# Optimization experiments

Hardware: AMD Instinct MI355X
Metric: run time of the kernel (lower is better)

## Reference

```python
import jax, jax.numpy as jnp
import numpy as np

B, S, IN, OUT, H, M = 16, 512, 512, 512, 8, 4
HF = OUT // H  # head_feats = 64


def setup_inputs() -> dict:
    key = jax.random.key(0)
    ks = jax.random.split(key, 12)
    std = 0.02
    queries = jax.random.normal(ks[0], (B, S, IN), jnp.float32)
    keys = jax.random.normal(ks[1], (B, S, IN), jnp.float32)
    timespans = jax.random.uniform(ks[2], (B, S), jnp.float32)
    # causal mask tiled over heads*batch, matching [H*B, S, S] score shape
    attention_masks = jnp.broadcast_to(jnp.tril(jnp.ones((S, S), jnp.float32)), (H * B, S, S))
    event_marks = jax.random.uniform(ks[3], (H * B, 1, S, M), jnp.float32)
    Wq = std * jax.random.normal(ks[4], (IN, OUT), jnp.float32)
    Wk = std * jax.random.normal(ks[5], (IN, OUT), jnp.float32)
    Wv = std * jax.random.normal(ks[6], (IN, OUT), jnp.float32)
    Wt = std * jax.random.normal(ks[7], (IN, OUT), jnp.float32)
    Wi = std * jax.random.normal(ks[8], (HF + 1, M * HF), jnp.float32)  # fc_i weight
    bi = jnp.zeros((M * HF,), jnp.float32)                               # fc_i bias
    weight_i = std * jax.random.normal(ks[9], (M, HF), jnp.float32)
    scale_i = jnp.zeros((M,), jnp.float32)
    return {"queries": queries, "keys": keys, "timespans": timespans,
            "attention_masks": attention_masks, "event_marks": event_marks,
            "Wq": Wq, "Wk": Wk, "Wv": Wv, "Wt": Wt, "Wi": Wi, "bi": bi,
            "weight_i": weight_i, "scale_i": scale_i}


def reference(queries, keys, timespans, attention_masks, event_marks,
              Wq, Wk, Wv, Wt, Wi, bi, weight_i, scale_i):
    # torch's cat(chunk(X, H, dim=2), dim=0) == [B,S,H,HF] -> [H,B,S,HF] -> flat h*B+b
    def split_heads(X):
        return X.reshape(B, S, H, HF).transpose(2, 0, 1, 3)  # [H,B,S,HF]

    Q = split_heads(queries @ Wq)
    K = split_heads(keys @ Wk)
    V = split_heads(keys @ Wv)
    T = split_heads(keys @ Wt)

    scores = jnp.einsum('hbqf,hbkf->hbqk', Q, K) / jnp.sqrt(jnp.float32(OUT))
    mask = attention_masks.reshape(H, B, S, S)
    scores = jnp.where(mask == 0.0, jnp.float32(-2 ** 32 + 1), scores)
    attn = jax.nn.softmax(scores, axis=-1)  # [H,B,Sq,Sk]

    E = jnp.einsum('hbqk,hbkf->hbqf', attn, T)  # events fed to intensity net

    # --- Hawkes intensities ---
    ts = jnp.broadcast_to(timespans[None, :, :, None], (H, B, S, 1))
    mu = jax.nn.sigmoid(jnp.concatenate([E, ts], axis=-1) @ Wi + bi)  # [H,B,S,M*HF]
    mu = mu.reshape(H, B, S, M, HF)  # chunk over marks along feature dim
    scale = jnp.exp(scale_i)  # [M]
    lam = jnp.einsum('hbsmf,mf->hbsm', mu, weight_i) / scale
    lam = scale * jnp.log1p(jnp.exp(lam))  # scaled softplus, [H,B,S,M]

    # mark_inty[h,b,q,k] = sum_m lam[h,b,q,m] * event_marks[h,b,k,m]
    em = event_marks.reshape(H, B, S, M)
    mark_inty = jnp.einsum('hbqm,hbkm->hbqk', lam, em)

    out = jnp.einsum('hbqk,hbkf->hbqf', attn * mark_inty, V)
    out = out.transpose(1, 2, 0, 3).reshape(B, S, OUT) + queries[..., :OUT]
    all_mark_inty = lam.reshape(H * B, S, M)
    return out, all_mark_inty
```

## Files before the change

kernel.cpp:

```cpp
#include <hip/hip_runtime.h>
#include <math.h>

typedef __attribute__((ext_vector_type(8))) short short8;
typedef __attribute__((ext_vector_type(4))) float f32x4;

static __device__ __forceinline__ unsigned short f2bf(float f) {
  unsigned int u = __float_as_uint(f);
  u += 0x7FFFu + ((u >> 16) & 1u);
  return (unsigned short)(u >> 16);
}

static __device__ __forceinline__ void cp16(void* lds, const void* g) {
  __builtin_amdgcn_global_load_lds((const __attribute__((address_space(1))) void*)g,
                                   (__attribute__((address_space(3))) void*)lds,
                                   16, 0, 0);
}

__global__ __launch_bounds__(256) void convert_k(
    const float* __restrict__ qin, const float* __restrict__ kin,
    const float* __restrict__ Wq, const float* __restrict__ Wk,
    const float* __restrict__ Wv, const float* __restrict__ Wt,
    const float* __restrict__ Wi,
    unsigned short* __restrict__ qbf, unsigned short* __restrict__ kbf,
    unsigned short* __restrict__ Wb, unsigned short* __restrict__ WiF)
{
  __shared__ unsigned short tr[64 * 68];
  const int blk = blockIdx.x, tid = threadIdx.x;
  if (blk < 8192) {
    const float* src = (blk < 4096) ? qin : kin;
    unsigned short* dst = (blk < 4096) ? qbf : kbf;
    int i = ((blk & 4095) * 256 + tid) * 4;
    float4 v = *(const float4*)(src + i);
    ushort4 o;
    o.x = f2bf(v.x); o.y = f2bf(v.y); o.z = f2bf(v.z); o.w = f2bf(v.w);
    *(ushort4*)(dst + i) = o;
  } else if (blk < 8448) {
    int t = blk - 8192;
    int which = t >> 6, tile = t & 63;
    int r0 = (tile >> 3) << 6, c0 = (tile & 7) << 6;
    const float* W = (which == 0) ? Wq : (which == 1) ? Wk : (which == 2) ? Wv : Wt;
    const int rr = tid >> 4, cc = (tid & 15) << 2;
#pragma unroll
    for (int u = 0; u < 4; ++u) {
      int r = rr + u * 16;
      float4 v = *(const float4*)(W + (size_t)(r0 + r) * 512 + c0 + cc);
      tr[(cc + 0) * 68 + r] = f2bf(v.x);
      tr[(cc + 1) * 68 + r] = f2bf(v.y);
      tr[(cc + 2) * 68 + r] = f2bf(v.z);
      tr[(cc + 3) * 68 + r] = f2bf(v.w);
    }
    __syncthreads();
    unsigned short* dst = Wb + which * 262144;
#pragma unroll
    for (int u = 0; u < 4; ++u) {
      int c = rr + u * 16;
      ushort4 o = *(const ushort4*)&tr[c * 68 + cc];
      *(ushort4*)(dst + (size_t)(c0 + c) * 512 + r0 + cc) = o;
    }
  } else {
    int e = (blk - 8448) * 256 + tid;
    int j = e & 7, ll = (e >> 3) & 63, r = e >> 9;
    int kk = r % 3, nt = r / 3;
    int col = nt * 16 + (ll & 15);
    int k = kk * 32 + (ll >> 4) * 8 + j;
    float val = (k < 64) ? Wi[k * 256 + col] : ((k == 64) ? Wi[16384 + col] : 0.0f);
    WiF[e] = f2bf(val);
  }
}

__global__ __launch_bounds__(256) void proj_mfma(
    const unsigned short* __restrict__ qin_bf, const unsigned short* __restrict__ kin_bf,
    const unsigned short* __restrict__ Wb,
    unsigned short* __restrict__ Qg, unsigned short* __restrict__ Kg,
    unsigned short* __restrict__ Vt, unsigned short* __restrict__ Tt)
{
  const int which = blockIdx.z;
  const unsigned short* A = (which == 0) ? qin_bf : kin_bf;
  const unsigned short* W = Wb + which * 262144;
  const int row0 = blockIdx.x * 128;
  const int col0 = blockIdx.y * 128;
  const int tid = threadIdx.x;
  const int wv = tid >> 6, l = tid & 63;
  const int quad = l >> 4, lc = l & 15;
  const int wm = wv >> 1, wn = wv & 1;

  __shared__ unsigned short Asm[128 * 32];
  __shared__ unsigned short Bsm[128 * 32];

  f32x4 acc[4][4] = {};
  const int c0 = tid, c1 = tid + 256;

  for (int k0 = 0; k0 < 512; k0 += 32) {
    __syncthreads();
    cp16(&Asm[c0 * 8], A + (size_t)(row0 + (c0 >> 2)) * 512 + k0 + (c0 & 3) * 8);
    cp16(&Asm[c1 * 8], A + (size_t)(row0 + (c1 >> 2)) * 512 + k0 + (c1 & 3) * 8);
    cp16(&Bsm[c0 * 8], W + (size_t)(col0 + (c0 >> 2)) * 512 + k0 + (c0 & 3) * 8);
    cp16(&Bsm[c1 * 8], W + (size_t)(col0 + (c1 >> 2)) * 512 + k0 + (c1 & 3) * 8);
    __syncthreads();
    short8 a[4], b[4];
#pragma unroll
    for (int mi = 0; mi < 4; ++mi)
      a[mi] = *(const short8*)&Asm[(wm * 64 + mi * 16 + lc) * 32 + quad * 8];
#pragma unroll
    for (int nj = 0; nj < 4; ++nj)
      b[nj] = *(const short8*)&Bsm[(wn * 64 + nj * 16 + lc) * 32 + quad * 8];
#pragma unroll
    for (int mi = 0; mi < 4; ++mi)
#pragma unroll
      for (int nj = 0; nj < 4; ++nj)
        acc[mi][nj] = __builtin_amdgcn_mfma_f32_16x16x32_bf16(a[mi], b[nj], acc[mi][nj], 0, 0, 0);
  }

  const int h = (col0 >> 6) + wn;
  const int bidx = row0 >> 9;
  const int hb = h * 16 + bidx;
  if (which < 2) {
    unsigned short* C = (which == 0) ? Qg : Kg;
    const float os = (which == 0) ? 0.044194173824159216f : 1.0f;
#pragma unroll
    for (int mi = 0; mi < 4; ++mi) {
      int sbase = (row0 & 511) + wm * 64 + mi * 16 + quad * 4;
#pragma unroll
      for (int nj = 0; nj < 4; ++nj) {
        size_t base = (size_t)hb * 32768 + (size_t)sbase * 64 + nj * 16 + lc;
#pragma unroll
        for (int reg = 0; reg < 4; ++reg)
          C[base + (size_t)reg * 64] = f2bf(acc[mi][nj][reg] * os);
      }
    }
  } else {
    unsigned short* C = (which == 2) ? Vt : Tt;
    unsigned short* scr = wn ? Bsm : Asm;
    const int sb = (row0 & 511) + wm * 64;
    __syncthreads();
#pragma unroll
    for (int round = 0; round < 2; ++round) {
      if (wm == round) {
#pragma unroll
        for (int mi = 0; mi < 4; ++mi)
#pragma unroll
          for (int nj = 0; nj < 4; ++nj)
#pragma unroll
            for (int reg = 0; reg < 4; ++reg) {
              int f = nj * 16 + lc, s = mi * 16 + quad * 4 + reg;
              int g = (s >> 3) ^ (f & 7);
              scr[f * 64 + g * 8 + (s & 7)] = f2bf(acc[mi][nj][reg]);
            }
#pragma unroll
        for (int it = 0; it < 8; ++it) {
          int fl = it * 8 + (l >> 3);
          int gg = (l & 7) ^ (fl & 7);
          short8 v = *(const short8*)&scr[fl * 64 + gg * 8];
          *(short8*)(C + (size_t)hb * 32768 + (size_t)fl * 512 + sb + (l & 7) * 8) = v;
        }
      }
      __syncthreads();
    }
  }
}

__global__ __launch_bounds__(256, 3) void attn_fused(
    const unsigned short* __restrict__ Qg, const unsigned short* __restrict__ Kg,
    const unsigned short* __restrict__ Vtg, const unsigned short* __restrict__ Ttg,
    const unsigned short* __restrict__ WiF,
    const float* __restrict__ bi, const float* __restrict__ wim,
    const float* __restrict__ sci, const float* __restrict__ tsp,
    const float* __restrict__ em, const float* __restrict__ queries,
    float* __restrict__ out, float* __restrict__ lamout)
{
  const int hb = blockIdx.x;
  const int qt = 7 - blockIdx.y;
  const int q0 = qt << 6;
  const int tid = threadIdx.x, wv = tid >> 6, l = tid & 63;
  const int quad = l >> 4, lc = l & 15;
  const int xg = lc & 7;

  __shared__ unsigned short Qs[4096];
  __shared__ unsigned short Ks[4096];
  __shared__ unsigned short TVs[4096];
  __shared__ unsigned short Wl[4][1536];
  __shared__ float emS[256];

  const int e1 = tid + 256;
  const int sr0 = tid >> 3, sg0 = (tid & 7) ^ (sr0 & 7);
  const int sr1 = e1 >> 3,  sg1 = (e1 & 7) ^ (sr1 & 7);
  const int sqk0 = sr0 * 64 + sg0 * 8,  sqk1 = sr1 * 64 + sg1 * 8;
  const int stv0 = sr0 * 512 + sg0 * 8, stv1 = sr1 * 512 + sg1 * 8;

  const int gqbase = q0 + wv * 16 + quad * 4;

  const unsigned short* Qbase = Qg + (size_t)hb * 32768 + q0 * 64;
  cp16(&Qs[tid * 8], Qbase + sqk0);
  cp16(&Qs[e1 * 8], Qbase + sqk1);

  f32x4 Eacc[4] = {};
  float lsum[4] = {0.f, 0.f, 0.f, 0.f};

  for (int kt = 0; kt <= qt; ++kt) {
    const int k0 = kt << 6;
    __syncthreads();
    const unsigned short* Kbase = Kg + (size_t)hb * 32768 + k0 * 64;
    cp16(&Ks[tid * 8], Kbase + sqk0);
    cp16(&Ks[e1 * 8], Kbase + sqk1);
    const unsigned short* Tbase = Ttg + (size_t)hb * 32768 + k0;
    cp16(&TVs[tid * 8], Tbase + stv0);
    cp16(&TVs[e1 * 8], Tbase + stv1);
    __syncthreads();

    f32x4 sc[4] = {};
#pragma unroll
    for (int kk = 0; kk < 2; ++kk) {
      short8 a = *(const short8*)&Qs[(wv * 16 + lc) * 64 + ((kk * 4 + quad) ^ xg) * 8];
#pragma unroll
      for (int nj = 0; nj < 4; ++nj) {
        short8 b = *(const short8*)&Ks[(nj * 16 + lc) * 64 + ((kk * 4 + quad) ^ xg) * 8];
        sc[nj] = __builtin_amdgcn_mfma_f32_16x16x32_bf16(a, b, sc[nj], 0, 0, 0);
      }
    }
    const bool diag = (kt == qt);
#pragma unroll
    for (int nj = 0; nj < 4; ++nj) {
      int col = nj * 16 + lc;
#pragma unroll
      for (int reg = 0; reg < 4; ++reg) {
        float pv = __expf(sc[nj][reg]);
        if (diag && (k0 + col) > (gqbase + reg)) pv = 0.0f;
        lsum[reg] += pv;
        int row = quad * 4 + reg;
        int gp = (nj * 2 + (lc >> 3)) ^ (row & 7);
        Wl[wv][row * 96 + gp * 8 + (lc & 7)] = f2bf(pv);
      }
    }
#pragma unroll
    for (int kk = 0; kk < 2; ++kk) {
      short8 a = *(const short8*)&Wl[wv][lc * 96 + ((kk * 4 + quad) ^ xg) * 8];
#pragma unroll
      for (int fj = 0; fj < 4; ++fj) {
        short8 b = *(const short8*)&TVs[(fj * 16 + lc) * 64 + ((kk * 4 + quad) ^ xg) * 8];
        Eacc[fj] = __builtin_amdgcn_mfma_f32_16x16x32_bf16(a, b, Eacc[fj], 0, 0, 0);
      }
    }
  }

  float inv[4];
#pragma unroll
  for (int reg = 0; reg < 4; ++reg) {
    float s = lsum[reg];
#pragma unroll
    for (int off = 1; off < 16; off <<= 1) s += __shfl_xor(s, off);
    inv[reg] = 1.0f / s;
  }

#pragma unroll
  for (int reg = 0; reg < 4; ++reg) {
    int row = quad * 4 + reg;
    unsigned short* rp = &Wl[wv][row * 96];
#pragma unroll
    for (int fj = 0; fj < 4; ++fj) {
      int gp = (fj * 2 + (lc >> 3)) ^ (row & 7);
      rp[gp * 8 + (lc & 7)] = f2bf(Eacc[fj][reg] * inv[reg]);
    }
    float tsv = (lc == 0) ? tsp[(hb & 15) * 512 + gqbase + reg] : 0.0f;
    int gt = 8 + ((lc >> 3) ^ (row & 3));
    rp[gt * 8 + (lc & 7)] = f2bf(tsv);
    int gz = 8 + ((2 + (lc >> 3)) ^ (row & 3));
    rp[gz * 8 + (lc & 7)] = 0;
  }

  short8 ia[3];
  ia[0] = *(const short8*)&Wl[wv][lc * 96 + ((0 + quad) ^ xg) * 8];
  ia[1] = *(const short8*)&Wl[wv][lc * 96 + ((4 + quad) ^ xg) * 8];
  ia[2] = *(const short8*)&Wl[wv][lc * 96 + (8 + (quad ^ (lc & 3))) * 8];
  float lam4[4][4] = {};
#pragma unroll
  for (int nt = 0; nt < 16; ++nt) {
    f32x4 iacc = {};
#pragma unroll
    for (int kk = 0; kk < 3; ++kk) {
      short8 b = *(const short8*)(WiF + ((nt * 3 + kk) * 64 + l) * 8);
      iacc = __builtin_amdgcn_mfma_f32_16x16x32_bf16(ia[kk], b, iacc, 0, 0, 0);
    }
    float bvv = bi[nt * 16 + lc];
    float wmv = wim[nt * 16 + lc];
#pragma unroll
    for (int reg = 0; reg < 4; ++reg) {
      float mu = 1.0f / (1.0f + __expf(-(iacc[reg] + bvv)));
      lam4[reg][nt >> 2] += mu * wmv;
    }
  }
#pragma unroll
  for (int m = 0; m < 4; ++m) {
    float scv = __expf(sci[m]);
#pragma unroll
    for (int reg = 0; reg < 4; ++reg) {
      float s = lam4[reg][m];
#pragma unroll
      for (int off = 1; off < 16; off <<= 1) s += __shfl_xor(s, off);
      float z = s / scv;
      float sp = (z > 20.0f) ? z : log1pf(__expf(z));
      lam4[reg][m] = scv * sp;
    }
  }
  if (lc < 4) {
#pragma unroll
    for (int reg = 0; reg < 4; ++reg) {
      float v = (lc == 0) ? lam4[reg][0] : (lc == 1) ? lam4[reg][1]
              : (lc == 2) ? lam4[reg][2] : lam4[reg][3];
      lamout[((size_t)hb * 512 + gqbase + reg) * 4 + lc] = v;
    }
  }

  f32x4 Oacc[4] = {};
  for (int kt = 0; kt <= qt; ++kt) {
    const int k0 = kt << 6;
    __syncthreads();
    const unsigned short* Kbase = Kg + (size_t)hb * 32768 + k0 * 64;
    cp16(&Ks[tid * 8], Kbase + sqk0);
    cp16(&Ks[e1 * 8], Kbase + sqk1);
    const unsigned short* Vbase = Vtg + (size_t)hb * 32768 + k0;
    cp16(&TVs[tid * 8], Vbase + stv0);
    cp16(&TVs[e1 * 8], Vbase + stv1);
    emS[tid] = em[(size_t)hb * 2048 + k0 * 4 + tid];
    __syncthreads();

    f32x4 sc[4] = {};
#pragma unroll
    for (int kk = 0; kk < 2; ++kk) {
      short8 a = *(const short8*)&Qs[(wv * 16 + lc) * 64 + ((kk * 4 + quad) ^ xg) * 8];
#pragma unroll
      for (int nj = 0; nj < 4; ++nj) {
        short8 b = *(const short8*)&Ks[(nj * 16 + lc) * 64 + ((kk * 4 + quad) ^ xg) * 8];
        sc[nj] = __builtin_amdgcn_mfma_f32_16x16x32_bf16(a, b, sc[nj], 0, 0, 0);
      }
    }
    const bool diag = (kt == qt);
#pragma unroll
    for (int nj = 0; nj < 4; ++nj) {
      int col = nj * 16 + lc;
      float4 emv = *(const float4*)&emS[col * 4];
#pragma unroll
      for (int reg = 0; reg < 4; ++reg) {
        float pv = (diag && (k0 + col) > (gqbase + reg))
                       ? 0.0f : __expf(sc[nj][reg]) * inv[reg];
        float mk = lam4[reg][0] * emv.x + lam4[reg][1] * emv.y +
                   lam4[reg][2] * emv.z + lam4[reg][3] * emv.w;
        int row = quad * 4 + reg;
        int gp = (nj * 2 + (lc >> 3)) ^ (row & 7);
        Wl[wv][row * 96 + gp * 8 + (lc & 7)] = f2bf(pv * mk);
      }
    }
#pragma unroll
    for (int kk = 0; kk < 2; ++kk) {
      short8 a = *(const short8*)&Wl[wv][lc * 96 + ((kk * 4 + quad) ^ xg) * 8];
#pragma unroll
      for (int fj = 0; fj < 4; ++fj) {
        short8 b = *(const short8*)&TVs[(fj * 16 + lc) * 64 + ((kk * 4 + quad) ^ xg) * 8];
        Oacc[fj] = __builtin_amdgcn_mfma_f32_16x16x32_bf16(a, b, Oacc[fj], 0, 0, 0);
      }
    }
  }

  const int h = hb >> 4, bidx = hb & 15;
#pragma unroll
  for (int reg = 0; reg < 4; ++reg) {
    size_t o = (size_t)bidx * 262144 + (size_t)(gqbase + reg) * 512 + h * 64 + lc;
#pragma unroll
    for (int fj = 0; fj < 4; ++fj)
      out[o + fj * 16] = Oacc[fj][reg] + queries[o + fj * 16];
  }
}

extern "C" void kernel_launch(void* const* d_in, const int* in_sizes, int n_in,
                              void* d_out, int out_size, void* d_ws, size_t ws_size,
                              hipStream_t stream)
{
  (void)in_sizes; (void)n_in; (void)out_size; (void)ws_size;
  const float* queries = (const float*)d_in[0];
  const float* keys    = (const float*)d_in[1];
  const float* tsp     = (const float*)d_in[2];
  const float* em      = (const float*)d_in[4];
  const float* Wq      = (const float*)d_in[5];
  const float* Wk      = (const float*)d_in[6];
  const float* Wv      = (const float*)d_in[7];
  const float* Wt      = (const float*)d_in[8];
  const float* Wi      = (const float*)d_in[9];
  const float* bi      = (const float*)d_in[10];
  const float* wim     = (const float*)d_in[11];
  const float* sci     = (const float*)d_in[12];
  float* out = (float*)d_out;

  char* w = (char*)d_ws;
  unsigned short* Qg     = (unsigned short*)(w + 0);
  unsigned short* Kg     = (unsigned short*)(w + 8388608);
  unsigned short* Vt     = (unsigned short*)(w + 16777216);
  unsigned short* Tt     = (unsigned short*)(w + 25165824);
  unsigned short* qin_bf = (unsigned short*)(w + 33554432);
  unsigned short* kin_bf = (unsigned short*)(w + 41943040);
  unsigned short* Wb     = (unsigned short*)(w + 50331648);
  unsigned short* WiF    = (unsigned short*)(w + 52428800);

  convert_k<<<8544, 256, 0, stream>>>(queries, keys, Wq, Wk, Wv, Wt, Wi,
                                      qin_bf, kin_bf, Wb, WiF);
  proj_mfma<<<dim3(64, 4, 4), 256, 0, stream>>>(qin_bf, kin_bf, Wb, Qg, Kg, Vt, Tt);
  attn_fused<<<dim3(128, 8), 256, 0, stream>>>(Qg, Kg, Vt, Tt, WiF, bi, wim, sci,
                                               tsp, em, queries, out,
                                               out + 4194304);
}
```

Before: 319.4 us.

## Enlarge attention query tile to 128 rows with double-buffered K/T/V loads

The fused attention kernel now handles 128 query rows per block, two 16-row tiles per wave, so each K/T/V tile loaded into LDS serves twice as many queries. Q fragments are kept in registers, and K/T/V/em tiles are double-buffered so the next tile's async load overlaps the current tile's compute, cutting one barrier per iteration. The grid halves and blocks are ordered largest-first to balance causal work. In exchange, LDS use and register pressure grow (launch bounds drop to 2 blocks per SM), fewer blocks are in flight, and diagonal masking is now checked on every tile.

```diff
diff --git a/kernel.cpp b/kernel.cpp
--- a/kernel.cpp
+++ b/kernel.cpp
@@ -159,7 +159,7 @@
   }
 }
 
-__global__ __launch_bounds__(256, 3) void attn_fused(
+__global__ __launch_bounds__(256, 2) void attn_fused(
     const unsigned short* __restrict__ Qg, const unsigned short* __restrict__ Kg,
     const unsigned short* __restrict__ Vtg, const unsigned short* __restrict__ Ttg,
     const unsigned short* __restrict__ WiF,
@@ -169,17 +169,19 @@
     float* __restrict__ out, float* __restrict__ lamout)
 {
   const int hb = blockIdx.x;
-  const int qt = 7 - blockIdx.y;
-  const int q0 = qt << 6;
+  const int y = blockIdx.y;
+  const int qb = (y == 0) ? 3 : (y == 1) ? 2 : (y == 2) ? 0 : 1;
+  const int q0 = qb << 7;
+  const int kts = 2 * qb + 2;
   const int tid = threadIdx.x, wv = tid >> 6, l = tid & 63;
   const int quad = l >> 4, lc = l & 15;
   const int xg = lc & 7;
 
-  __shared__ unsigned short Qs[4096];
-  __shared__ unsigned short Ks[4096];
-  __shared__ unsigned short TVs[4096];
-  __shared__ unsigned short Wl[4][1536];
-  __shared__ float emS[256];
+  __shared__ unsigned short Qs[8192];
+  __shared__ unsigned short Ks[2][4096];
+  __shared__ unsigned short TVs[2][4096];
+  __shared__ unsigned short Wl[4][3072];
+  __shared__ float emS[2][256];
 
   const int e1 = tid + 256;
   const int sr0 = tid >> 3, sg0 = (tid & 7) ^ (sr0 & 7);
@@ -187,186 +189,238 @@
   const int sqk0 = sr0 * 64 + sg0 * 8,  sqk1 = sr1 * 64 + sg1 * 8;
   const int stv0 = sr0 * 512 + sg0 * 8, stv1 = sr1 * 512 + sg1 * 8;
 
-  const int gqbase = q0 + wv * 16 + quad * 4;
+  const unsigned short* KgB = Kg + (size_t)hb * 32768;
+  const unsigned short* TgB = Ttg + (size_t)hb * 32768;
+  const unsigned short* VgB = Vtg + (size_t)hb * 32768;
 
   const unsigned short* Qbase = Qg + (size_t)hb * 32768 + q0 * 64;
-  cp16(&Qs[tid * 8], Qbase + sqk0);
-  cp16(&Qs[e1 * 8], Qbase + sqk1);
-
-  f32x4 Eacc[4] = {};
-  float lsum[4] = {0.f, 0.f, 0.f, 0.f};
-
-  for (int kt = 0; kt <= qt; ++kt) {
+#pragma unroll
+  for (int u = 0; u < 4; ++u) {
+    int e = tid + u * 256;
+    int r = e >> 3, g = (e & 7) ^ (r & 7);
+    cp16(&Qs[e * 8], Qbase + r * 64 + g * 8);
+  }
+  cp16(&Ks[0][tid * 8], KgB + sqk0);
+  cp16(&Ks[0][e1 * 8], KgB + sqk1);
+  cp16(&TVs[0][tid * 8], TgB + stv0);
+  cp16(&TVs[0][e1 * 8], TgB + stv1);
+  __syncthreads();
+
+  short8 aq[2][2];
+#pragma unroll
+  for (int rt = 0; rt < 2; ++rt)
+#pragma unroll
+    for (int kk = 0; kk < 2; ++kk)
+      aq[rt][kk] = *(const short8*)&Qs[(wv * 32 + rt * 16 + lc) * 64 + ((kk * 4 + quad) ^ xg) * 8];
+
+  f32x4 Eacc[2][4] = {};
+  float lsum[2][4] = {};
+
+  for (int kt = 0; kt < kts; ++kt) {
+    const int cur = kt & 1, nxt = cur ^ 1;
     const int k0 = kt << 6;
-    __syncthreads();
-    const unsigned short* Kbase = Kg + (size_t)hb * 32768 + k0 * 64;
-    cp16(&Ks[tid * 8], Kbase + sqk0);
-    cp16(&Ks[e1 * 8], Kbase + sqk1);
-    const unsigned short* Tbase = Ttg + (size_t)hb * 32768 + k0;
-    cp16(&TVs[tid * 8], Tbase + stv0);
-    cp16(&TVs[e1 * 8], Tbase + stv1);
-    __syncthreads();
-
-    f32x4 sc[4] = {};
-#pragma unroll
-    for (int kk = 0; kk < 2; ++kk) {
-      short8 a = *(const short8*)&Qs[(wv * 16 + lc) * 64 + ((kk * 4 + quad) ^ xg) * 8];
+    if (kt + 1 < kts) {
+      const int k1 = (kt + 1) << 6;
+      cp16(&Ks[nxt][tid * 8], KgB + k1 * 64 + sqk0);
+      cp16(&Ks[nxt][e1 * 8], KgB + k1 * 64 + sqk1);
+      cp16(&TVs[nxt][tid * 8], TgB + k1 + stv0);
+      cp16(&TVs[nxt][e1 * 8], TgB + k1 + stv1);
+    }
+    f32x4 sc[2][4] = {};
+#pragma unroll
+    for (int kk = 0; kk < 2; ++kk)
 #pragma unroll
       for (int nj = 0; nj < 4; ++nj) {
-        short8 b = *(const short8*)&Ks[(nj * 16 + lc) * 64 + ((kk * 4 + quad) ^ xg) * 8];
-        sc[nj] = __builtin_amdgcn_mfma_f32_16x16x32_bf16(a, b, sc[nj], 0, 0, 0);
-      }
-    }
-    const bool diag = (kt == qt);
-#pragma unroll
-    for (int nj = 0; nj < 4; ++nj) {
-      int col = nj * 16 + lc;
+        short8 b = *(const short8*)&Ks[cur][(nj * 16 + lc) * 64 + ((kk * 4 + quad) ^ xg) * 8];
+        sc[0][nj] = __builtin_amdgcn_mfma_f32_16x16x32_bf16(aq[0][kk], b, sc[0][nj], 0, 0, 0);
+        sc[1][nj] = __builtin_amdgcn_mfma_f32_16x16x32_bf16(aq[1][kk], b, sc[1][nj], 0, 0, 0);
+      }
+#pragma unroll
+    for (int rt = 0; rt < 2; ++rt) {
+      const int gq = q0 + wv * 32 + rt * 16 + quad * 4;
+#pragma unroll
+      for (int nj = 0; nj < 4; ++nj) {
+        int col = nj * 16 + lc;
+#pragma unroll
+        for (int reg = 0; reg < 4; ++reg) {
+          float pv = __expf(sc[rt][nj][reg]);
+          if (k0 + col > gq + reg) pv = 0.0f;
+          lsum[rt][reg] += pv;
+          int row = rt * 16 + quad * 4 + reg;
+          int gp = (nj * 2 + (lc >> 3)) ^ (row & 7);
+          Wl[wv][row * 96 + gp * 8 + (lc & 7)] = f2bf(pv);
+        }
+      }
+    }
+#pragma unroll
+    for (int rt = 0; rt < 2; ++rt)
+#pragma unroll
+      for (int kk = 0; kk < 2; ++kk) {
+        short8 a = *(const short8*)&Wl[wv][(rt * 16 + lc) * 96 + ((kk * 4 + quad) ^ xg) * 8];
+#pragma unroll
+        for (int fj = 0; fj < 4; ++fj) {
+          short8 b = *(const short8*)&TVs[cur][(fj * 16 + lc) * 64 + ((kk * 4 + quad) ^ xg) * 8];
+          Eacc[rt][fj] = __builtin_amdgcn_mfma_f32_16x16x32_bf16(a, b, Eacc[rt][fj], 0, 0, 0);
+        }
+      }
+    __syncthreads();
+  }
+
+  float inv[2][4];
+#pragma unroll
+  for (int rt = 0; rt < 2; ++rt)
+#pragma unroll
+    for (int reg = 0; reg < 4; ++reg) {
+      float s = lsum[rt][reg];
+#pragma unroll
+      for (int off = 1; off < 16; off <<= 1) s += __shfl_xor(s, off);
+      inv[rt][reg] = 1.0f / s;
+    }
+
+#pragma unroll
+  for (int rt = 0; rt < 2; ++rt)
+#pragma unroll
+    for (int reg = 0; reg < 4; ++reg) {
+      int row = rt * 16 + quad * 4 + reg;
+      int gq = q0 + wv * 32 + rt * 16 + quad * 4;
+      unsigned short* rp = &Wl[wv][row * 96];
+#pragma unroll
+      for (int fj = 0; fj < 4; ++fj) {
+        int gp = (fj * 2 + (lc >> 3)) ^ (row & 7);
+        rp[gp * 8 + (lc & 7)] = f2bf(Eacc[rt][fj][reg] * inv[rt][reg]);
+      }
+      float tsv = (lc == 0) ? tsp[(hb & 15) * 512 + gq + reg] : 0.0f;
+      int gt = 8 + ((lc >> 3) ^ (row & 3));
+      rp[gt * 8 + (lc & 7)] = f2bf(tsv);
+      int gz = 8 + ((2 + (lc >> 3)) ^ (row & 3));
+      rp[gz * 8 + (lc & 7)] = 0;
+    }
+
+  float lam4[2][4][4];
+#pragma unroll
+  for (int rt = 0; rt < 2; ++rt) {
+    short8 ia[3];
+    ia[0] = *(const short8*)&Wl[wv][(rt * 16 + lc) * 96 + ((0 + quad) ^ xg) * 8];
+    ia[1] = *(const short8*)&Wl[wv][(rt * 16 + lc) * 96 + ((4 + quad) ^ xg) * 8];
+    ia[2] = *(const short8*)&Wl[wv][(rt * 16 + lc) * 96 + (8 + (quad ^ (lc & 3))) * 8];
+    float lac[4][4] = {};
+#pragma unroll
+    for (int nt = 0; nt < 16; ++nt) {
+      f32x4 iacc = {};
+#pragma unroll
+      for (int kk = 0; kk < 3; ++kk) {
+        short8 b = *(const short8*)(WiF + ((nt * 3 + kk) * 64 + l) * 8);
+        iacc = __builtin_amdgcn_mfma_f32_16x16x32_bf16(ia[kk], b, iacc, 0, 0, 0);
+      }
+      float bvv = bi[nt * 16 + lc];
+      float wmv = wim[nt * 16 + lc];
 #pragma unroll
       for (int reg = 0; reg < 4; ++reg) {
-        float pv = __expf(sc[nj][reg]);
-        if (diag && (k0 + col) > (gqbase + reg)) pv = 0.0f;
-        lsum[reg] += pv;
-        int row = quad * 4 + reg;
-        int gp = (nj * 2 + (lc >> 3)) ^ (row & 7);
-        Wl[wv][row * 96 + gp * 8 + (lc & 7)] = f2bf(pv);
-      }
-    }
-#pragma unroll
-    for (int kk = 0; kk < 2; ++kk) {
-      short8 a = *(const short8*)&Wl[wv][lc * 96 + ((kk * 4 + quad) ^ xg) * 8];
-#pragma unroll
-      for (int fj = 0; fj < 4; ++fj) {
-        short8 b = *(const short8*)&TVs[(fj * 16 + lc) * 64 + ((kk * 4 + quad) ^ xg) * 8];
-        Eacc[fj] = __builtin_amdgcn_mfma_f32_16x16x32_bf16(a, b, Eacc[fj], 0, 0, 0);
-      }
-    }
-  }
-
-  float inv[4];
-#pragma unroll
-  for (int reg = 0; reg < 4; ++reg) {
-    float s = lsum[reg];
-#pragma unroll
-    for (int off = 1; off < 16; off <<= 1) s += __shfl_xor(s, off);
-    inv[reg] = 1.0f / s;
-  }
-
-#pragma unroll
-  for (int reg = 0; reg < 4; ++reg) {
-    int row = quad * 4 + reg;
-    unsigned short* rp = &Wl[wv][row * 96];
-#pragma unroll
-    for (int fj = 0; fj < 4; ++fj) {
-      int gp = (fj * 2 + (lc >> 3)) ^ (row & 7);
-      rp[gp * 8 + (lc & 7)] = f2bf(Eacc[fj][reg] * inv[reg]);
-    }
-    float tsv = (lc == 0) ? tsp[(hb & 15) * 512 + gqbase + reg] : 0.0f;
-    int gt = 8 + ((lc >> 3) ^ (row & 3));
-    rp[gt * 8 + (lc & 7)] = f2bf(tsv);
-    int gz = 8 + ((2 + (lc >> 3)) ^ (row & 3));
-    rp[gz * 8 + (lc & 7)] = 0;
-  }
-
-  short8 ia[3];
-  ia[0] = *(const short8*)&Wl[wv][lc * 96 + ((0 + quad) ^ xg) * 8];
-  ia[1] = *(const short8*)&Wl[wv][lc * 96 + ((4 + quad) ^ xg) * 8];
-  ia[2] = *(const short8*)&Wl[wv][lc * 96 + (8 + (quad ^ (lc & 3))) * 8];
-  float lam4[4][4] = {};
-#pragma unroll
-  for (int nt = 0; nt < 16; ++nt) {
-    f32x4 iacc = {};
-#pragma unroll
-    for (int kk = 0; kk < 3; ++kk) {
-      short8 b = *(const short8*)(WiF + ((nt * 3 + kk) * 64 + l) * 8);
-      iacc = __builtin_amdgcn_mfma_f32_16x16x32_bf16(ia[kk], b, iacc, 0, 0, 0);
-    }
-    float bvv = bi[nt * 16 + lc];
-    float wmv = wim[nt * 16 + lc];
+        float mu = 1.0f / (1.0f + __expf(-(iacc[reg] + bvv)));
+        lac[reg][nt >> 2] += mu * wmv;
+      }
+    }
+#pragma unroll
+    for (int m = 0; m < 4; ++m) {
+      float scv = __expf(sci[m]);
+#pragma unroll
+      for (int reg = 0; reg < 4; ++reg) {
+        float s = lac[reg][m];
+#pragma unroll
+        for (int off = 1; off < 16; off <<= 1) s += __shfl_xor(s, off);
+        float z = s / scv;
+        float sp = (z > 20.0f) ? z : log1pf(__expf(z));
+        lam4[rt][reg][m] = scv * sp;
+      }
+    }
+    if (lc < 4) {
+      int gq = q0 + wv * 32 + rt * 16 + quad * 4;
+#pragma unroll
+      for (int reg = 0; reg < 4; ++reg) {
+        float v = (lc == 0) ? lam4[rt][reg][0] : (lc == 1) ? lam4[rt][reg][1]
+                : (lc == 2) ? lam4[rt][reg][2] : lam4[rt][reg][3];
+        lamout[((size_t)hb * 512 + gq + reg) * 4 + lc] = v;
+      }
+    }
+#pragma unroll
+    for (int reg = 0; reg < 4; ++reg)
+#pragma unroll
+      for (int m = 0; m < 4; ++m)
+        lam4[rt][reg][m] *= inv[rt][reg];
+  }
+
+  cp16(&Ks[0][tid * 8], KgB + sqk0);
+  cp16(&Ks[0][e1 * 8], KgB + sqk1);
+  cp16(&TVs[0][tid * 8], VgB + stv0);
+  cp16(&TVs[0][e1 * 8], VgB + stv1);
+  emS[0][tid] = em[(size_t)hb * 2048 + tid];
+  __syncthreads();
+
+  f32x4 Oacc[2][4] = {};
+  for (int kt = 0; kt < kts; ++kt) {
+    const int cur = kt & 1, nxt = cur ^ 1;
+    const int k0 = kt << 6;
+    if (kt + 1 < kts) {
+      const int k1 = (kt + 1) << 6;
+      cp16(&Ks[nxt][tid * 8], KgB + k1 * 64 + sqk0);
+      cp16(&Ks[nxt][e1 * 8], KgB + k1 * 64 + sqk1);
+      cp16(&TVs[nxt][tid * 8], VgB + k1 + stv0);
+      cp16(&TVs[nxt][e1 * 8], VgB + k1 + stv1);
+      emS[nxt][tid] = em[(size_t)hb * 2048 + k1 * 4 + tid];
+    }
+    f32x4 sc[2][4] = {};
+#pragma unroll
+    for (int kk = 0; kk < 2; ++kk)
+#pragma unroll
+      for (int nj = 0; nj < 4; ++nj) {
+        short8 b = *(const short8*)&Ks[cur][(nj * 16 + lc) * 64 + ((kk * 4 + quad) ^ xg) * 8];
+        sc[0][nj] = __builtin_amdgcn_mfma_f32_16x16x32_bf16(aq[0][kk], b, sc[0][nj], 0, 0, 0);
+        sc[1][nj] = __builtin_amdgcn_mfma_f32_16x16x32_bf16(aq[1][kk], b, sc[1][nj], 0, 0, 0);
+      }
+#pragma unroll
+    for (int rt = 0; rt < 2; ++rt) {
+      const int gq = q0 + wv * 32 + rt * 16 + quad * 4;
+#pragma unroll
+      for (int nj = 0; nj < 4; ++nj) {
+        int col = nj * 16 + lc;
+        float4 emv = *(const float4*)&emS[cur][col * 4];
+#pragma unroll
+        for (int reg = 0; reg < 4; ++reg) {
+          float pv = __expf(sc[rt][nj][reg]);
+          if (k0 + col > gq + reg) pv = 0.0f;
+          float mk = lam4[rt][reg][0] * emv.x + lam4[rt][reg][1] * emv.y +
+                     lam4[rt][reg][2] * emv.z + lam4[rt][reg][3] * emv.w;
+          int row = rt * 16 + quad * 4 + reg;
+          int gp = (nj * 2 + (lc >> 3)) ^ (row & 7);
+          Wl[wv][row * 96 + gp * 8 + (lc & 7)] = f2bf(pv * mk);
+        }
+      }
+    }
+#pragma unroll
+    for (int rt = 0; rt < 2; ++rt)
+#pragma unroll
+      for (int kk = 0; kk < 2; ++kk) {
+        short8 a = *(const short8*)&Wl[wv][(rt * 16 + lc) * 96 + ((kk * 4 + quad) ^ xg) * 8];
+#pragma unroll
+        for (int fj = 0; fj < 4; ++fj) {
+          short8 b = *(const short8*)&TVs[cur][(fj * 16 + lc) * 64 + ((kk * 4 + quad) ^ xg) * 8];
+          Oacc[rt][fj] = __builtin_amdgcn_mfma_f32_16x16x32_bf16(a, b, Oacc[rt][fj], 0, 0, 0);
+        }
+      }
+    __syncthreads();
+  }
+
+  const int h = hb >> 4, bidx = hb & 15;
+#pragma unroll
+  for (int rt = 0; rt < 2; ++rt) {
+    const int gq = q0 + wv * 32 + rt * 16 + quad * 4;
 #pragma unroll
     for (int reg = 0; reg < 4; ++reg) {
-      float mu = 1.0f / (1.0f + __expf(-(iacc[reg] + bvv)));
-      lam4[reg][nt >> 2] += mu * wmv;
-    }
-  }
-#pragma unroll
-  for (int m = 0; m < 4; ++m) {
-    float scv = __expf(sci[m]);
-#pragma unroll
-    for (int reg = 0; reg < 4; ++reg) {
-      float s = lam4[reg][m];
-#pragma unroll
-      for (int off = 1; off < 16; off <<= 1) s += __shfl_xor(s, off);
-      float z = s / scv;
-      float sp = (z > 20.0f) ? z : log1pf(__expf(z));
-      lam4[reg][m] = scv * sp;
-    }
-  }
-  if (lc < 4) {
-#pragma unroll
-    for (int reg = 0; reg < 4; ++reg) {
-      float v = (lc == 0) ? lam4[reg][0] : (lc == 1) ? lam4[reg][1]
-              : (lc == 2) ? lam4[reg][2] : lam4[reg][3];
-      lamout[((size_t)hb * 512 + gqbase + reg) * 4 + lc] = v;
-    }
-  }
-
-  f32x4 Oacc[4] = {};
-  for (int kt = 0; kt <= qt; ++kt) {
-    const int k0 = kt << 6;
-    __syncthreads();
-    const unsigned short* Kbase = Kg + (size_t)hb * 32768 + k0 * 64;
-    cp16(&Ks[tid * 8], Kbase + sqk0);
-    cp16(&Ks[e1 * 8], Kbase + sqk1);
-    const unsigned short* Vbase = Vtg + (size_t)hb * 32768 + k0;
-    cp16(&TVs[tid * 8], Vbase + stv0);
-    cp16(&TVs[e1 * 8], Vbase + stv1);
-    emS[tid] = em[(size_t)hb * 2048 + k0 * 4 + tid];
-    __syncthreads();
-
-    f32x4 sc[4] = {};
-#pragma unroll
-    for (int kk = 0; kk < 2; ++kk) {
-      short8 a = *(const short8*)&Qs[(wv * 16 + lc) * 64 + ((kk * 4 + quad) ^ xg) * 8];
-#pragma unroll
-      for (int nj = 0; nj < 4; ++nj) {
-        short8 b = *(const short8*)&Ks[(nj * 16 + lc) * 64 + ((kk * 4 + quad) ^ xg) * 8];
-        sc[nj] = __builtin_amdgcn_mfma_f32_16x16x32_bf16(a, b, sc[nj], 0, 0, 0);
-      }
-    }
-    const bool diag = (kt == qt);
-#pragma unroll
-    for (int nj = 0; nj < 4; ++nj) {
-      int col = nj * 16 + lc;
-      float4 emv = *(const float4*)&emS[col * 4];
-#pragma unroll
-      for (int reg = 0; reg < 4; ++reg) {
-        float pv = (diag && (k0 + col) > (gqbase + reg))
-                       ? 0.0f : __expf(sc[nj][reg]) * inv[reg];
-        float mk = lam4[reg][0] * emv.x + lam4[reg][1] * emv.y +
-                   lam4[reg][2] * emv.z + lam4[reg][3] * emv.w;
-        int row = quad * 4 + reg;
-        int gp = (nj * 2 + (lc >> 3)) ^ (row & 7);
-        Wl[wv][row * 96 + gp * 8 + (lc & 7)] = f2bf(pv * mk);
-      }
-    }
-#pragma unroll
-    for (int kk = 0; kk < 2; ++kk) {
-      short8 a = *(const short8*)&Wl[wv][lc * 96 + ((kk * 4 + quad) ^ xg) * 8];
-#pragma unroll
-      for (int fj = 0; fj < 4; ++fj) {
-        short8 b = *(const short8*)&TVs[(fj * 16 + lc) * 64 + ((kk * 4 + quad) ^ xg) * 8];
-        Oacc[fj] = __builtin_amdgcn_mfma_f32_16x16x32_bf16(a, b, Oacc[fj], 0, 0, 0);
-      }
-    }
-  }
-
-  const int h = hb >> 4, bidx = hb & 15;
-#pragma unroll
-  for (int reg = 0; reg < 4; ++reg) {
-    size_t o = (size_t)bidx * 262144 + (size_t)(gqbase + reg) * 512 + h * 64 + lc;
-#pragma unroll
-    for (int fj = 0; fj < 4; ++fj)
-      out[o + fj * 16] = Oacc[fj][reg] + queries[o + fj * 16];
+      size_t o = (size_t)bidx * 262144 + (size_t)(gq + reg) * 512 + h * 64 + lc;
+#pragma unroll
+      for (int fj = 0; fj < 4; ++fj)
+        out[o + fj * 16] = Oacc[rt][fj][reg] + queries[o + fj * 16];
+    }
   }
 }
 
@@ -402,7 +456,7 @@
   convert_k<<<8544, 256, 0, stream>>>(queries, keys, Wq, Wk, Wv, Wt, Wi,
                                       qin_bf, kin_bf, Wb, WiF);
   proj_mfma<<<dim3(64, 4, 4), 256, 0, stream>>>(qin_bf, kin_bf, Wb, Qg, Kg, Vt, Tt);
-  attn_fused<<<dim3(128, 8), 256, 0, stream>>>(Qg, Kg, Vt, Tt, WiF, bi, wim, sci,
+  attn_fused<<<dim3(128, 4), 256, 0, stream>>>(Qg, Kg, Vt, Tt, WiF, bi, wim, sci,
                                                tsp, em, queries, out,
                                                out + 4194304);
 }
```

Measured after the change: 313.1 us. 1.02x faster.
